# Performance work log

Measured on AMD Instinct MI355X. Metric: run time of the kernel, lower is better.

Reference implementation:

```python
import jax, jax.numpy as jnp
import numpy as np

N0, N1, N2, N3 = 1_000_000, 300_000, 80_000, 30_000
CIN, C = 4, 64  # in_channels, INIT_DIM / PLANES[0]
K = 27          # 3x3x3 octree kernel
EPS = 1e-5      # BatchNorm eps


def octree_conv(x, neigh, W):
    """Octree sparse conv as gather + GEMM.
    x: [Nin, Cin], neigh: [Nout, K] int indices into x, W: [K, Cin, Cout].
    """
    g = x[neigh]                              # [Nout, K, Cin] irregular gather
    return jnp.einsum('nkc,kcd->nd', g, W)    # [Nout, Cout]


def batchnorm(x, gamma, beta):
    # BatchNorm1d in training mode: batch stats over node dim, biased variance
    m = jnp.mean(x, axis=0)
    v = jnp.var(x, axis=0)
    return (x - m) * jax.lax.rsqrt(v + EPS) * gamma + beta


def setup_inputs() -> dict:
    key = jax.random.key(0)
    ks = jax.random.split(key, 16)
    s = 0.05
    return {
        'x': jax.random.normal(ks[0], (N0, CIN), jnp.float32),
        'neigh_stem': jax.random.randint(ks[1], (N1, K), 0, N0, jnp.int32),
        'pool_child': jax.random.randint(ks[2], (N2, 8), 0, N1, jnp.int32),
        'neigh_ds': jax.random.randint(ks[3], (N3, K), 0, N2, jnp.int32),
        'neigh_res': jax.random.randint(ks[4], (N3, K), 0, N3, jnp.int32),
        'W_stem': jax.random.normal(ks[5], (K, CIN, C), jnp.float32) * s,
        'g_stem': jnp.ones((C,), jnp.float32),
        'b_stem': jnp.zeros((C,), jnp.float32),
        'W1': jax.random.normal(ks[6], (K, C, C), jnp.float32) * s,
        'g1': jnp.ones((C,), jnp.float32),
        'b1': jnp.zeros((C,), jnp.float32),
        'W2': jax.random.normal(ks[7], (K, C, C), jnp.float32) * s,
        'g2': jnp.ones((C,), jnp.float32),
        'b2': jnp.zeros((C,), jnp.float32),
        'Wd': jax.random.normal(ks[8], (K, C, C), jnp.float32) * s,
        'gd': jnp.ones((C,), jnp.float32),
        'bd': jnp.zeros((C,), jnp.float32),
    }


def reference(x, neigh_stem, pool_child, neigh_ds, neigh_res,
              W_stem, g_stem, b_stem, W1, g1, b1, W2, g2, b2, Wd, gd, bd):
    # StemLayer: conv(s2) -> BN -> ReLU -> OctreeMaxPool
    h = jax.nn.relu(batchnorm(octree_conv(x, neigh_stem, W_stem), g_stem, b_stem))  # [N1, C]
    h = jnp.max(h[pool_child], axis=1)                                              # [N2, C]
    # ResBlock stride=2 (layer1, blocks=1)
    out = jax.nn.relu(batchnorm(octree_conv(h, neigh_ds, W1), g1, b1))              # [N3, C]
    out = batchnorm(octree_conv(out, neigh_res, W2), g2, b2)                        # [N3, C]
    residual = batchnorm(octree_conv(h, neigh_ds, Wd), gd, bd)                      # DownSample shortcut
    return jax.nn.relu(out + residual)
```

## Files before the change

kernel.cpp:

```cpp
#include <hip/hip_runtime.h>

constexpr int CN0 = 1000000;
constexpr int CN1 = 300000;
constexpr int CN2 = 80000;
constexpr int CN3 = 30000;
constexpr float BN_EPS = 1e-5f;

typedef __attribute__((ext_vector_type(8))) short bf16x8;
typedef __attribute__((ext_vector_type(4))) float f32x4;

union FragU { uint4 u; bf16x8 b; };

__device__ __forceinline__ float2 bn_ab(float s, float q, float invn, float gamma, float beta) {
  float m = s * invn;
  float v = fmaf(q, invn, -m * m);
  float rstd = rsqrtf(v + BN_EPS);
  float a = gamma * rstd;
  float b = beta - m * a;
  return make_float2(a, b);
}

__device__ __forceinline__ unsigned short f2bf(float f) {
  unsigned u = __float_as_uint(f);
  u += 0x7FFFu + ((u >> 16) & 1u);
  return (unsigned short)(u >> 16);
}

__device__ __forceinline__ void sync_lds() {
  asm volatile("s_waitcnt lgkmcnt(0)" ::: "memory");
  __builtin_amdgcn_s_barrier();
  asm volatile("" ::: "memory");
}

__global__ __launch_bounds__(256) void k_prep_x(
    const float* __restrict__ x, unsigned int* __restrict__ xbf) {
  int i = blockIdx.x * 256 + threadIdx.x;
  if (i >= CN0) return;
  float4 v = *(const float4*)(x + i * 4);
  uint2 p;
  p.x = (unsigned)f2bf(v.x) | ((unsigned)f2bf(v.y) << 16);
  p.y = (unsigned)f2bf(v.z) | ((unsigned)f2bf(v.w) << 16);
  *(uint2*)(xbf + i * 2) = p;
}

__global__ __launch_bounds__(256) void k_prep_stem(
    const float* __restrict__ W, unsigned short* __restrict__ Wt) {
  int f = blockIdx.x * 256 + threadIdx.x;
  if (f >= 8192) return;
  int e = f & 7, lane = (f >> 3) & 63, nf = (f >> 9) & 3, ks = f >> 11;
  int k = ks * 32 + (lane >> 4) * 8 + e;
  int d = nf * 16 + (lane & 15);
  Wt[f] = (k < 108) ? f2bf(W[k * 64 + d]) : (unsigned short)0;
}

__global__ __launch_bounds__(256) void k_prep_dual(
    const float* __restrict__ W1, const float* __restrict__ Wd,
    unsigned short* __restrict__ Wf) {
  int f = blockIdx.x * 256 + threadIdx.x;
  if (f >= 27 * 8192) return;
  int tap = f >> 13, r = f & 8191;
  int ks1 = (r >> 12) & 1, nfg = (r >> 9) & 7, lane = (r >> 3) & 63, e = r & 7;
  int cin = ks1 * 32 + (lane >> 4) * 8 + e;
  int d = nfg * 16 + (lane & 15);
  float v = (d < 64) ? W1[(tap * 64 + cin) * 64 + d]
                     : Wd[(tap * 64 + cin) * 64 + (d - 64)];
  Wf[f] = f2bf(v);
}

__global__ __launch_bounds__(256) void k_prep_res(
    const float* __restrict__ W2, unsigned short* __restrict__ Wf) {
  int f = blockIdx.x * 256 + threadIdx.x;
  if (f >= 27 * 4096) return;
  int tap = f >> 12, r = f & 4095;
  int ks1 = (r >> 11) & 1, nfg = (r >> 9) & 3, lane = (r >> 3) & 63, e = r & 7;
  int cin = ks1 * 32 + (lane >> 4) * 8 + e;
  int d = nfg * 16 + (lane & 15);
  Wf[f] = f2bf(W2[(tap * 64 + cin) * 64 + d]);
}

__global__ __launch_bounds__(256) void k_stem_mfma(
    const unsigned short* __restrict__ xbf, const int* __restrict__ neigh,
    const unsigned short* __restrict__ Wf, unsigned short* __restrict__ y1,
    float* __restrict__ stats) {
  __shared__ __align__(16) uint4 Bb[1024];
  const int tid = threadIdx.x;
  const int lane = tid & 63;
  const int wv = tid >> 6;
  const int l15 = lane & 15, lq = lane >> 4;
  const int g0 = blockIdx.x * 2;

  uint4 wreg[4];
  {
    const uint4* Ws = (const uint4*)Wf;
#pragma unroll
    for (int j = 0; j < 4; ++j) wreg[j] = Ws[tid + j * 256];
  }

  int idx0[8], idx1[8];
#define LDIDX(g, dst)                                                      \
  {                                                                        \
    int node_ = (g)*64 + wv * 16 + l15;                                    \
    bool rowok_ = node_ < CN1;                                             \
    const int* nb_ = neigh + node_ * 27;                                   \
    _Pragma("unroll") for (int ks_ = 0; ks_ < 4; ++ks_) {                  \
      int tap0_ = ks_ * 8 + lq * 2;                                        \
      dst[ks_ * 2] = (rowok_ && tap0_ < 27) ? nb_[tap0_] : -1;             \
      dst[ks_ * 2 + 1] = (rowok_ && tap0_ + 1 < 27) ? nb_[tap0_ + 1] : -1; \
    }                                                                      \
  }
#define GATHER(idx, frag)                                                  \
  {                                                                        \
    _Pragma("unroll") for (int ks_ = 0; ks_ < 4; ++ks_) {                  \
      uint2 v0_ = {0u, 0u}, v1_ = {0u, 0u};                                \
      if (idx[ks_ * 2] >= 0)                                               \
        v0_ = *(const uint2*)(xbf + idx[ks_ * 2] * 4);                     \
      if (idx[ks_ * 2 + 1] >= 0)                                           \
        v1_ = *(const uint2*)(xbf + idx[ks_ * 2 + 1] * 4);                 \
      frag[ks_].u.x = v0_.x; frag[ks_].u.y = v0_.y;                        \
      frag[ks_].u.z = v1_.x; frag[ks_].u.w = v1_.y;                        \
    }                                                                      \
  }

  LDIDX(g0 + 0, idx0);
  LDIDX(g0 + 1, idx1);
  FragU fA[4], fB[4];
  GATHER(idx0, fA);
  GATHER(idx1, fB);

#pragma unroll
  for (int j = 0; j < 4; ++j) Bb[tid + j * 256] = wreg[j];
  sync_lds();

  float sacc[4] = {0.f, 0.f, 0.f, 0.f};
  float qacc[4] = {0.f, 0.f, 0.f, 0.f};

#pragma unroll
  for (int t = 0; t < 2; ++t) {
    FragU* cur = t ? fB : fA;
    f32x4 acc[4] = {};
#pragma unroll
    for (int ks = 0; ks < 4; ++ks) {
#pragma unroll
      for (int nf = 0; nf < 4; ++nf) {
        bf16x8 b = *(const bf16x8*)&Bb[(ks * 4 + nf) * 64 + lane];
        acc[nf] = __builtin_amdgcn_mfma_f32_16x16x32_bf16(cur[ks].b, b,
                                                          acc[nf], 0, 0, 0);
      }
    }
    int n0 = (g0 + t) * 64 + wv * 16;
#pragma unroll
    for (int nf = 0; nf < 4; ++nf) {
      int c = nf * 16 + l15;
#pragma unroll
      for (int r = 0; r < 4; ++r) {
        int row = n0 + lq * 4 + r;
        float v = acc[nf][r];
        if (row < CN1) y1[row * 64 + c] = f2bf(v);
        sacc[nf] += v;
        qacc[nf] = fmaf(v, v, qacc[nf]);
      }
    }
  }
#undef LDIDX
#undef GATHER

  sync_lds();
  float* S = (float*)Bb;
#pragma unroll
  for (int nf = 0; nf < 4; ++nf) {
    float s = sacc[nf], q = qacc[nf];
    s += __shfl_xor(s, 16); s += __shfl_xor(s, 32);
    q += __shfl_xor(q, 16); q += __shfl_xor(q, 32);
    if (lane < 16) {
      S[wv * 64 + nf * 16 + lane] = s;
      S[256 + wv * 64 + nf * 16 + lane] = q;
    }
  }
  __syncthreads();
  if (tid < 64) {
    float s = S[tid] + S[64 + tid] + S[128 + tid] + S[192 + tid];
    float q = S[256 + tid] + S[320 + tid] + S[384 + tid] + S[448 + tid];
    atomicAdd(&stats[tid], s);
    atomicAdd(&stats[64 + tid], q);
  }
}

__global__ __launch_bounds__(256) void k_pool(
    const unsigned int* __restrict__ y1, const int* __restrict__ child,
    const float* __restrict__ stats, const float* __restrict__ gamma,
    const float* __restrict__ beta, unsigned int* __restrict__ h2) {
  const int tid = threadIdx.x;
  const int wd = tid & 31;
  const int n = blockIdx.x * 8 + (tid >> 5);
  const int c0 = wd * 2, c1 = c0 + 1;
  const int* crow = child + n * 8;
  int ch[8];
#pragma unroll
  for (int j = 0; j < 8; ++j) ch[j] = crow[j];
  unsigned vv[8];
#pragma unroll
  for (int j = 0; j < 8; ++j) vv[j] = y1[ch[j] * 32 + wd];

  float2 ab0 = bn_ab(stats[c0], stats[64 + c0], 1.0f / CN1, gamma[c0], beta[c0]);
  float2 ab1 = bn_ab(stats[c1], stats[64 + c1], 1.0f / CN1, gamma[c1], beta[c1]);
  float mx0 = -INFINITY, mn0 = INFINITY, mx1 = -INFINITY, mn1 = INFINITY;
#pragma unroll
  for (int j = 0; j < 8; ++j) {
    float v0 = __uint_as_float(vv[j] << 16);
    float v1 = __uint_as_float(vv[j] & 0xFFFF0000u);
    mx0 = fmaxf(mx0, v0); mn0 = fminf(mn0, v0);
    mx1 = fmaxf(mx1, v1); mn1 = fminf(mn1, v1);
  }
  float t0 = (ab0.x > 0.f) ? fmaf(ab0.x, mx0, ab0.y) : fmaf(ab0.x, mn0, ab0.y);
  float t1 = (ab1.x > 0.f) ? fmaf(ab1.x, mx1, ab1.y) : fmaf(ab1.x, mn1, ab1.y);
  unsigned o = (unsigned)f2bf(fmaxf(t0, 0.f)) |
               ((unsigned)f2bf(fmaxf(t1, 0.f)) << 16);
  h2[n * 32 + wd] = o;
}

template <int OUTC>
__global__ __launch_bounds__(OUTC * 2) void k_mconv(
    const unsigned short* __restrict__ src, const int* __restrict__ neigh,
    const unsigned short* __restrict__ Wf, float* __restrict__ out,
    float* __restrict__ stats, int M) {
  constexpr int CG = OUTC / 64;
  constexpr int PT = CG * 512;
  constexpr int K1 = 4 * CG;

  const int tid = threadIdx.x;
  const int lane = tid & 63;
  const int w = tid >> 6;
  const int ng = w & 1, cg = w >> 1;
  const int l15 = lane & 15, lq = lane >> 4;
  const int node = blockIdx.x * 32 + ng * 16 + l15;
  const bool ok = node < M;
  const int* myn = neigh + node * 27;
  const uint4* WfU = (const uint4*)Wf;
  const int cg4 = cg * 4;

  int i0 = -1, i1 = -1, i2 = -1, i3 = -1, i4 = -1, i5 = -1, i6 = -1,
      i7 = -1, i8 = -1, i9 = -1, i10 = -1, i11 = -1, i12 = -1, i13 = -1,
      i14 = -1, i15 = -1, i16 = -1, i17 = -1, i18 = -1, i19 = -1, i20 = -1,
      i21 = -1, i22 = -1, i23 = -1, i24 = -1, i25 = -1, i26 = -1;
  if (ok) {
    i0 = myn[0];   i1 = myn[1];   i2 = myn[2];   i3 = myn[3];
    i4 = myn[4];   i5 = myn[5];   i6 = myn[6];   i7 = myn[7];
    i8 = myn[8];   i9 = myn[9];   i10 = myn[10]; i11 = myn[11];
    i12 = myn[12]; i13 = myn[13]; i14 = myn[14]; i15 = myn[15];
    i16 = myn[16]; i17 = myn[17]; i18 = myn[18]; i19 = myn[19];
    i20 = myn[20]; i21 = myn[21]; i22 = myn[22]; i23 = myn[23];
    i24 = myn[24]; i25 = myn[25]; i26 = myn[26];
  }

  FragU a0l, a0h, a1l, a1h, a2l, a2h;
  FragU qa0, qa1, qa2, qa3, qa4, qa5, qa6, qa7;
  FragU qb0, qb1, qb2, qb3, qb4, qb5, qb6, qb7;
  f32x4 acc0 = {0.f, 0.f, 0.f, 0.f};
  f32x4 acc1 = {0.f, 0.f, 0.f, 0.f};
  f32x4 acc2 = {0.f, 0.f, 0.f, 0.f};
  f32x4 acc3 = {0.f, 0.f, 0.f, 0.f};

#define GATH2(AL, AH, ix)                                                  \
  {                                                                        \
    int ix_ = (ix);                                                        \
    if (ix_ >= 0) {                                                        \
      const char* bp_ = (const char*)src + (size_t)ix_ * 128 + lq * 16;    \
      AL.u = *(const uint4*)bp_;                                           \
      AH.u = *(const uint4*)(bp_ + 64);                                    \
    } else {                                                               \
      AL.u = uint4{0u, 0u, 0u, 0u};                                        \
      AH.u = uint4{0u, 0u, 0u, 0u};                                        \
    }                                                                      \
  }

#define LDB(QP, k)                                                         \
  {                                                                        \
    const uint4* bp_ = WfU + ((k)*PT + cg4 * 64 + lane);                   \
    (QP##0).u = bp_[0];                                                    \
    (QP##1).u = bp_[64];                                                   \
    (QP##2).u = bp_[128];                                                  \
    (QP##3).u = bp_[192];                                                  \
    (QP##4).u = bp_[K1 * 64];                                              \
    (QP##5).u = bp_[K1 * 64 + 64];                                         \
    (QP##6).u = bp_[K1 * 64 + 128];                                        \
    (QP##7).u = bp_[K1 * 64 + 192];                                        \
  }

#define MM(AP, QP)                                                            \
  acc0 = __builtin_amdgcn_mfma_f32_16x16x32_bf16((AP##l).b, (QP##0).b, acc0, 0, 0, 0); \
  acc0 = __builtin_amdgcn_mfma_f32_16x16x32_bf16((AP##h).b, (QP##4).b, acc0, 0, 0, 0); \
  acc1 = __builtin_amdgcn_mfma_f32_16x16x32_bf16((AP##l).b, (QP##1).b, acc1, 0, 0, 0); \
  acc1 = __builtin_amdgcn_mfma_f32_16x16x32_bf16((AP##h).b, (QP##5).b, acc1, 0, 0, 0); \
  acc2 = __builtin_amdgcn_mfma_f32_16x16x32_bf16((AP##l).b, (QP##2).b, acc2, 0, 0, 0); \
  acc2 = __builtin_amdgcn_mfma_f32_16x16x32_bf16((AP##h).b, (QP##6).b, acc2, 0, 0, 0); \
  acc3 = __builtin_amdgcn_mfma_f32_16x16x32_bf16((AP##l).b, (QP##3).b, acc3, 0, 0, 0); \
  acc3 = __builtin_amdgcn_mfma_f32_16x16x32_bf16((AP##h).b, (QP##7).b, acc3, 0, 0, 0);

#define TAP(k, AP, QP, QN, INX)          \
  {                                      \
    if ((k) + 1 < 27) LDB(QN, (k) + 1)   \
    MM(AP, QP)                           \
    if ((k) + 3 < 27) GATH2(AP##l, AP##h, INX) \
  }

  GATH2(a0l, a0h, i0)
  GATH2(a1l, a1h, i1)
  GATH2(a2l, a2h, i2)
  LDB(qa, 0)

  TAP(0, a0, qa, qb, i3)
  TAP(1, a1, qb, qa, i4)
  TAP(2, a2, qa, qb, i5)
  TAP(3, a0, qb, qa, i6)
  TAP(4, a1, qa, qb, i7)
  TAP(5, a2, qb, qa, i8)
  TAP(6, a0, qa, qb, i9)
  TAP(7, a1, qb, qa, i10)
  TAP(8, a2, qa, qb, i11)
  TAP(9, a0, qb, qa, i12)
  TAP(10, a1, qa, qb, i13)
  TAP(11, a2, qb, qa, i14)
  TAP(12, a0, qa, qb, i15)
  TAP(13, a1, qb, qa, i16)
  TAP(14, a2, qa, qb, i17)
  TAP(15, a0, qb, qa, i18)
  TAP(16, a1, qa, qb, i19)
  TAP(17, a2, qb, qa, i20)
  TAP(18, a0, qa, qb, i21)
  TAP(19, a1, qb, qa, i22)
  TAP(20, a2, qa, qb, i23)
  TAP(21, a0, qb, qa, i24)
  TAP(22, a1, qa, qb, i25)
  TAP(23, a2, qb, qa, i26)
  TAP(24, a0, qa, qb, i0)
  TAP(25, a1, qb, qa, i0)
  TAP(26, a2, qa, qb, i0)
#undef TAP
#undef MM
#undef LDB
#undef GATH2

  const int rowbase = blockIdx.x * 32 + ng * 16 + lq * 4;
#pragma unroll
  for (int nf = 0; nf < 4; ++nf) {
    f32x4 a = (nf == 0) ? acc0 : (nf == 1) ? acc1 : (nf == 2) ? acc2 : acc3;
    int c = cg * 64 + nf * 16 + l15;
#pragma unroll
    for (int r = 0; r < 4; ++r) {
      int row = rowbase + r;
      if (row < M) out[row * OUTC + c] = a[r];
    }
  }

#pragma unroll
  for (int nf = 0; nf < 4; ++nf) {
    f32x4 a = (nf == 0) ? acc0 : (nf == 1) ? acc1 : (nf == 2) ? acc2 : acc3;
    float s = 0.f, q = 0.f;
#pragma unroll
    for (int r = 0; r < 4; ++r) {
      float v = a[r];
      s += v; q += v * v;
    }
    s += __shfl_xor(s, 16); s += __shfl_xor(s, 32);
    q += __shfl_xor(q, 16); q += __shfl_xor(q, 32);
    if (lane < 16) {
      int c = cg * 64 + nf * 16 + lane;
      atomicAdd(&stats[c], s);
      atomicAdd(&stats[OUTC + c], q);
    }
  }
}

__global__ __launch_bounds__(256) void k_bnrelu(
    const float* __restrict__ y2d, const float* __restrict__ stats,
    const float* __restrict__ gamma, const float* __restrict__ beta,
    unsigned short* __restrict__ out1) {
  int e = blockIdx.x * 256 + threadIdx.x;
  int i = e >> 6, c = e & 63;
  float2 ab = bn_ab(stats[c], stats[128 + c], 1.0f / CN3, gamma[c], beta[c]);
  out1[e] = f2bf(fmaxf(fmaf(ab.x, y2d[i * 128 + c], ab.y), 0.f));
}

__global__ __launch_bounds__(256) void k_final(
    const float* __restrict__ y3, const float* __restrict__ y2d,
    const float* __restrict__ stats2, const float* __restrict__ stats1d,
    const float* __restrict__ g2, const float* __restrict__ b2,
    const float* __restrict__ gd, const float* __restrict__ bd,
    float* __restrict__ dout) {
  int e = blockIdx.x * 256 + threadIdx.x;
  int i = e >> 6, c = e & 63;
  float2 ab2 = bn_ab(stats2[c], stats2[64 + c], 1.0f / CN3, g2[c], b2[c]);
  float2 abd =
      bn_ab(stats1d[64 + c], stats1d[192 + c], 1.0f / CN3, gd[c], bd[c]);
  float o = fmaf(ab2.x, y3[e], ab2.y) + fmaf(abd.x, y2d[i * 128 + 64 + c], abd.y);
  dout[e] = fmaxf(o, 0.f);
}

extern "C" void kernel_launch(void* const* d_in, const int* in_sizes, int n_in,
                              void* d_out, int out_size, void* d_ws,
                              size_t ws_size, hipStream_t stream) {
  const float* x = (const float*)d_in[0];
  const int* neigh_stem = (const int*)d_in[1];
  const int* pool_child = (const int*)d_in[2];
  const int* neigh_ds = (const int*)d_in[3];
  const int* neigh_res = (const int*)d_in[4];
  const float* W_stem = (const float*)d_in[5];
  const float* g_stem = (const float*)d_in[6];
  const float* b_stem = (const float*)d_in[7];
  const float* W1 = (const float*)d_in[8];
  const float* g1 = (const float*)d_in[9];
  const float* b1 = (const float*)d_in[10];
  const float* W2 = (const float*)d_in[11];
  const float* g2 = (const float*)d_in[12];
  const float* b2 = (const float*)d_in[13];
  const float* Wd = (const float*)d_in[14];
  const float* gd = (const float*)d_in[15];
  const float* bd = (const float*)d_in[16];
  float* out = (float*)d_out;
  float* ws = (float*)d_ws;

  unsigned short* y1bf = (unsigned short*)ws;
  float* y2d = ws;
  unsigned short* out1bf = (unsigned short*)(ws + 3840000);
  float* y3 = ws + 4800000;
  unsigned short* h2bf = (unsigned short*)(ws + 9600000);
  unsigned int* xbf = (unsigned int*)(ws + 12160000);
  unsigned short* Wst = (unsigned short*)(ws + 14160000);
  unsigned short* Wdual = (unsigned short*)(ws + 14164096);
  unsigned short* Wres = (unsigned short*)(ws + 14274688);
  float* stats = ws + 14329984;
  float* stats_stem = stats;
  float* stats_1d = stats + 128;
  float* stats_2 = stats + 384;

  hipMemsetAsync(stats, 0, 512 * sizeof(float), stream);

  k_prep_x<<<(CN0 + 255) / 256, 256, 0, stream>>>(x, xbf);
  k_prep_stem<<<(8192 + 255) / 256, 256, 0, stream>>>(W_stem, Wst);
  k_prep_dual<<<(27 * 8192 + 255) / 256, 256, 0, stream>>>(W1, Wd, Wdual);
  k_prep_res<<<(27 * 4096 + 255) / 256, 256, 0, stream>>>(W2, Wres);

  k_stem_mfma<<<2344, 256, 0, stream>>>(
      (const unsigned short*)xbf, neigh_stem, Wst, y1bf, stats_stem);
  k_pool<<<CN2 / 8, 256, 0, stream>>>((const unsigned int*)y1bf, pool_child,
                                      stats_stem, g_stem, b_stem,
                                      (unsigned int*)h2bf);
  k_mconv<128><<<(CN3 + 31) / 32, 256, 0, stream>>>(h2bf, neigh_ds, Wdual,
                                                    y2d, stats_1d, CN3);
  k_bnrelu<<<CN3 * 64 / 256, 256, 0, stream>>>(y2d, stats_1d, g1, b1, out1bf);
  k_mconv<64><<<(CN3 + 31) / 32, 128, 0, stream>>>(out1bf, neigh_res, Wres,
                                                   y3, stats_2, CN3);
  k_final<<<CN3 * 64 / 256, 256, 0, stream>>>(y3, y2d, stats_2, stats_1d, g2,
                                              b2, gd, bd, out);
}
```

Before: 292.4 us.

## Process more rows per block in stem and mconv, stage neighbor indices in LDS

The stem conv kernel now handles four 64-row groups per block instead of two, with a software pipeline that gathers the next group and loads indices two groups ahead while the current group computes. The weight tile is written straight into LDS at the start. The mconv kernel now covers 64 nodes per block with two accumulator sets, so each loaded weight fragment feeds twice as many MFMAs. Its neighbor indices are staged cooperatively in LDS rather than kept in 27 registers per thread. This halves the weight reloads and block count, at the cost of more registers, fewer blocks for latency hiding, and an LDS index read on every gather.

```diff
diff --git a/kernel.cpp b/kernel.cpp
--- a/kernel.cpp
+++ b/kernel.cpp
@@ -82,61 +82,65 @@
     const unsigned short* __restrict__ xbf, const int* __restrict__ neigh,
     const unsigned short* __restrict__ Wf, unsigned short* __restrict__ y1,
     float* __restrict__ stats) {
+  constexpr int T = 4;
   __shared__ __align__(16) uint4 Bb[1024];
   const int tid = threadIdx.x;
   const int lane = tid & 63;
   const int wv = tid >> 6;
   const int l15 = lane & 15, lq = lane >> 4;
-  const int g0 = blockIdx.x * 2;
-
-  uint4 wreg[4];
+  const int g0 = blockIdx.x * T;
+
   {
-    const uint4* Ws = (const uint4*)Wf;
-#pragma unroll
-    for (int j = 0; j < 4; ++j) wreg[j] = Ws[tid + j * 256];
-  }
-
-  int idx0[8], idx1[8];
-#define LDIDX(g, dst)                                                      \
-  {                                                                        \
-    int node_ = (g)*64 + wv * 16 + l15;                                    \
-    bool rowok_ = node_ < CN1;                                             \
-    const int* nb_ = neigh + node_ * 27;                                   \
-    _Pragma("unroll") for (int ks_ = 0; ks_ < 4; ++ks_) {                  \
-      int tap0_ = ks_ * 8 + lq * 2;                                        \
-      dst[ks_ * 2] = (rowok_ && tap0_ < 27) ? nb_[tap0_] : -1;             \
+    const uint4* Wsrc = (const uint4*)Wf;
+#pragma unroll
+    for (int j = 0; j < 4; ++j) Bb[tid + j * 256] = Wsrc[tid + j * 256];
+  }
+  __syncthreads();
+
+  int idxA[8], idxB[8];
+  FragU fragA[4], fragB[4];
+
+#define LDIDX(g, dst)                                                   \
+  {                                                                     \
+    int node_ = (g)*64 + wv * 16 + l15;                                 \
+    bool rowok_ = node_ < CN1;                                          \
+    const int* nb_ = neigh + node_ * 27;                                \
+    _Pragma("unroll") for (int ks_ = 0; ks_ < 4; ++ks_) {               \
+      int tap0_ = ks_ * 8 + lq * 2;                                     \
+      dst[ks_ * 2] = (rowok_ && tap0_ < 27) ? nb_[tap0_] : -1;          \
       dst[ks_ * 2 + 1] = (rowok_ && tap0_ + 1 < 27) ? nb_[tap0_ + 1] : -1; \
-    }                                                                      \
-  }
-#define GATHER(idx, frag)                                                  \
-  {                                                                        \
-    _Pragma("unroll") for (int ks_ = 0; ks_ < 4; ++ks_) {                  \
-      uint2 v0_ = {0u, 0u}, v1_ = {0u, 0u};                                \
-      if (idx[ks_ * 2] >= 0)                                               \
-        v0_ = *(const uint2*)(xbf + idx[ks_ * 2] * 4);                     \
-      if (idx[ks_ * 2 + 1] >= 0)                                           \
-        v1_ = *(const uint2*)(xbf + idx[ks_ * 2 + 1] * 4);                 \
-      frag[ks_].u.x = v0_.x; frag[ks_].u.y = v0_.y;                        \
-      frag[ks_].u.z = v1_.x; frag[ks_].u.w = v1_.y;                        \
-    }                                                                      \
-  }
-
-  LDIDX(g0 + 0, idx0);
-  LDIDX(g0 + 1, idx1);
-  FragU fA[4], fB[4];
-  GATHER(idx0, fA);
-  GATHER(idx1, fB);
-
-#pragma unroll
-  for (int j = 0; j < 4; ++j) Bb[tid + j * 256] = wreg[j];
-  sync_lds();
+    }                                                                   \
+  }
+
+#define GATHER(idx, frag)                                               \
+  {                                                                     \
+    _Pragma("unroll") for (int ks_ = 0; ks_ < 4; ++ks_) {               \
+      uint2 v0_ = {0u, 0u}, v1_ = {0u, 0u};                             \
+      if (idx[ks_ * 2] >= 0)                                            \
+        v0_ = *(const uint2*)(xbf + idx[ks_ * 2] * 4);                  \
+      if (idx[ks_ * 2 + 1] >= 0)                                        \
+        v1_ = *(const uint2*)(xbf + idx[ks_ * 2 + 1] * 4);              \
+      frag[ks_].u.x = v0_.x; frag[ks_].u.y = v0_.y;                     \
+      frag[ks_].u.z = v1_.x; frag[ks_].u.w = v1_.y;                     \
+    }                                                                   \
+  }
+
+  LDIDX(0 + g0, idxA);
+  GATHER(idxA, fragA);
+  LDIDX(1 + g0, idxB);
 
   float sacc[4] = {0.f, 0.f, 0.f, 0.f};
   float qacc[4] = {0.f, 0.f, 0.f, 0.f};
 
 #pragma unroll
-  for (int t = 0; t < 2; ++t) {
-    FragU* cur = t ? fB : fA;
+  for (int t = 0; t < T; ++t) {
+    FragU* cur = (t & 1) ? fragB : fragA;
+    FragU* nxt = (t & 1) ? fragA : fragB;
+    int* idn = (t & 1) ? idxA : idxB;
+    int* idn2 = (t & 1) ? idxB : idxA;
+    if (t + 1 < T) GATHER(idn, nxt);
+    if (t + 2 < T) LDIDX(g0 + t + 2, idn2);
+
     f32x4 acc[4] = {};
 #pragma unroll
     for (int ks = 0; ks < 4; ++ks) {
@@ -147,6 +151,7 @@
                                                           acc[nf], 0, 0, 0);
       }
     }
+
     int n0 = (g0 + t) * 64 + wv * 16;
 #pragma unroll
     for (int nf = 0; nf < 4; ++nf) {
@@ -164,7 +169,7 @@
 #undef LDIDX
 #undef GATHER
 
-  sync_lds();
+  __syncthreads();
   float* S = (float*)Bb;
 #pragma unroll
   for (int nf = 0; nf < 4; ++nf) {
@@ -224,41 +229,47 @@
     const unsigned short* __restrict__ Wf, float* __restrict__ out,
     float* __restrict__ stats, int M) {
   constexpr int CG = OUTC / 64;
+  constexpr int THREADS = OUTC * 2;
   constexpr int PT = CG * 512;
   constexpr int K1 = 4 * CG;
+  __shared__ int nlds[64 * 27];
 
   const int tid = threadIdx.x;
   const int lane = tid & 63;
   const int w = tid >> 6;
   const int ng = w & 1, cg = w >> 1;
   const int l15 = lane & 15, lq = lane >> 4;
-  const int node = blockIdx.x * 32 + ng * 16 + l15;
-  const bool ok = node < M;
-  const int* myn = neigh + node * 27;
   const uint4* WfU = (const uint4*)Wf;
   const int cg4 = cg * 4;
-
-  int i0 = -1, i1 = -1, i2 = -1, i3 = -1, i4 = -1, i5 = -1, i6 = -1,
-      i7 = -1, i8 = -1, i9 = -1, i10 = -1, i11 = -1, i12 = -1, i13 = -1,
-      i14 = -1, i15 = -1, i16 = -1, i17 = -1, i18 = -1, i19 = -1, i20 = -1,
-      i21 = -1, i22 = -1, i23 = -1, i24 = -1, i25 = -1, i26 = -1;
-  if (ok) {
-    i0 = myn[0];   i1 = myn[1];   i2 = myn[2];   i3 = myn[3];
-    i4 = myn[4];   i5 = myn[5];   i6 = myn[6];   i7 = myn[7];
-    i8 = myn[8];   i9 = myn[9];   i10 = myn[10]; i11 = myn[11];
-    i12 = myn[12]; i13 = myn[13]; i14 = myn[14]; i15 = myn[15];
-    i16 = myn[16]; i17 = myn[17]; i18 = myn[18]; i19 = myn[19];
-    i20 = myn[20]; i21 = myn[21]; i22 = myn[22]; i23 = myn[23];
-    i24 = myn[24]; i25 = myn[25]; i26 = myn[26];
-  }
-
-  FragU a0l, a0h, a1l, a1h, a2l, a2h;
+  const int offA = (ng * 32 + l15) * 27;
+  const int offB = offA + 16 * 27;
+
+  for (int e = tid; e < 64 * 27; e += THREADS) {
+    int row = blockIdx.x * 64 + e / 27;
+    nlds[e] = (row < M) ? neigh[row * 27 + e % 27] : -1;
+  }
+
+  FragU x0l, x0h, x1l, x1h, x2l, x2h;
+  FragU y0l, y0h, y1l, y1h, y2l, y2h;
   FragU qa0, qa1, qa2, qa3, qa4, qa5, qa6, qa7;
   FragU qb0, qb1, qb2, qb3, qb4, qb5, qb6, qb7;
-  f32x4 acc0 = {0.f, 0.f, 0.f, 0.f};
-  f32x4 acc1 = {0.f, 0.f, 0.f, 0.f};
-  f32x4 acc2 = {0.f, 0.f, 0.f, 0.f};
-  f32x4 acc3 = {0.f, 0.f, 0.f, 0.f};
+  f32x4 ca0 = {0.f, 0.f, 0.f, 0.f}, ca1 = {0.f, 0.f, 0.f, 0.f};
+  f32x4 ca2 = {0.f, 0.f, 0.f, 0.f}, ca3 = {0.f, 0.f, 0.f, 0.f};
+  f32x4 cb0 = {0.f, 0.f, 0.f, 0.f}, cb1 = {0.f, 0.f, 0.f, 0.f};
+  f32x4 cb2 = {0.f, 0.f, 0.f, 0.f}, cb3 = {0.f, 0.f, 0.f, 0.f};
+
+#define LDB(QP, k)                                                         \
+  {                                                                        \
+    const uint4* bp_ = WfU + ((k)*PT + cg4 * 64 + lane);                   \
+    (QP##0).u = bp_[0];                                                    \
+    (QP##1).u = bp_[64];                                                   \
+    (QP##2).u = bp_[128];                                                  \
+    (QP##3).u = bp_[192];                                                  \
+    (QP##4).u = bp_[K1 * 64];                                              \
+    (QP##5).u = bp_[K1 * 64 + 64];                                         \
+    (QP##6).u = bp_[K1 * 64 + 128];                                        \
+    (QP##7).u = bp_[K1 * 64 + 192];                                        \
+  }
 
 #define GATH2(AL, AH, ix)                                                  \
   {                                                                        \
@@ -273,93 +284,92 @@
     }                                                                      \
   }
 
-#define LDB(QP, k)                                                         \
-  {                                                                        \
-    const uint4* bp_ = WfU + ((k)*PT + cg4 * 64 + lane);                   \
-    (QP##0).u = bp_[0];                                                    \
-    (QP##1).u = bp_[64];                                                   \
-    (QP##2).u = bp_[128];                                                  \
-    (QP##3).u = bp_[192];                                                  \
-    (QP##4).u = bp_[K1 * 64];                                              \
-    (QP##5).u = bp_[K1 * 64 + 64];                                         \
-    (QP##6).u = bp_[K1 * 64 + 128];                                        \
-    (QP##7).u = bp_[K1 * 64 + 192];                                        \
-  }
-
-#define MM(AP, QP)                                                            \
-  acc0 = __builtin_amdgcn_mfma_f32_16x16x32_bf16((AP##l).b, (QP##0).b, acc0, 0, 0, 0); \
-  acc0 = __builtin_amdgcn_mfma_f32_16x16x32_bf16((AP##h).b, (QP##4).b, acc0, 0, 0, 0); \
-  acc1 = __builtin_amdgcn_mfma_f32_16x16x32_bf16((AP##l).b, (QP##1).b, acc1, 0, 0, 0); \
-  acc1 = __builtin_amdgcn_mfma_f32_16x16x32_bf16((AP##h).b, (QP##5).b, acc1, 0, 0, 0); \
-  acc2 = __builtin_amdgcn_mfma_f32_16x16x32_bf16((AP##l).b, (QP##2).b, acc2, 0, 0, 0); \
-  acc2 = __builtin_amdgcn_mfma_f32_16x16x32_bf16((AP##h).b, (QP##6).b, acc2, 0, 0, 0); \
-  acc3 = __builtin_amdgcn_mfma_f32_16x16x32_bf16((AP##l).b, (QP##3).b, acc3, 0, 0, 0); \
-  acc3 = __builtin_amdgcn_mfma_f32_16x16x32_bf16((AP##h).b, (QP##7).b, acc3, 0, 0, 0);
-
-#define TAP(k, AP, QP, QN, INX)          \
-  {                                      \
-    if ((k) + 1 < 27) LDB(QN, (k) + 1)   \
-    MM(AP, QP)                           \
-    if ((k) + 3 < 27) GATH2(AP##l, AP##h, INX) \
-  }
-
-  GATH2(a0l, a0h, i0)
-  GATH2(a1l, a1h, i1)
-  GATH2(a2l, a2h, i2)
+#define MMG(AL, AH, C0, C1, C2, C3, QP)                                       \
+  C0 = __builtin_amdgcn_mfma_f32_16x16x32_bf16((AL).b, (QP##0).b, C0, 0, 0, 0); \
+  C1 = __builtin_amdgcn_mfma_f32_16x16x32_bf16((AL).b, (QP##1).b, C1, 0, 0, 0); \
+  C2 = __builtin_amdgcn_mfma_f32_16x16x32_bf16((AL).b, (QP##2).b, C2, 0, 0, 0); \
+  C3 = __builtin_amdgcn_mfma_f32_16x16x32_bf16((AL).b, (QP##3).b, C3, 0, 0, 0); \
+  C0 = __builtin_amdgcn_mfma_f32_16x16x32_bf16((AH).b, (QP##4).b, C0, 0, 0, 0); \
+  C1 = __builtin_amdgcn_mfma_f32_16x16x32_bf16((AH).b, (QP##5).b, C1, 0, 0, 0); \
+  C2 = __builtin_amdgcn_mfma_f32_16x16x32_bf16((AH).b, (QP##6).b, C2, 0, 0, 0); \
+  C3 = __builtin_amdgcn_mfma_f32_16x16x32_bf16((AH).b, (QP##7).b, C3, 0, 0, 0);
+
+#define TAP(k, XL, XH, YL, YH, QP, QN)                 \
+  {                                                    \
+    if ((k) + 1 < 27) LDB(QN, (k) + 1)                 \
+    MMG(XL, XH, ca0, ca1, ca2, ca3, QP)                \
+    MMG(YL, YH, cb0, cb1, cb2, cb3, QP)                \
+    if ((k) + 3 < 27) {                                \
+      GATH2(XL, XH, nlds[offA + (k) + 3])              \
+      GATH2(YL, YH, nlds[offB + (k) + 3])              \
+    }                                                  \
+  }
+
   LDB(qa, 0)
-
-  TAP(0, a0, qa, qb, i3)
-  TAP(1, a1, qb, qa, i4)
-  TAP(2, a2, qa, qb, i5)
-  TAP(3, a0, qb, qa, i6)
-  TAP(4, a1, qa, qb, i7)
-  TAP(5, a2, qb, qa, i8)
-  TAP(6, a0, qa, qb, i9)
-  TAP(7, a1, qb, qa, i10)
-  TAP(8, a2, qa, qb, i11)
-  TAP(9, a0, qb, qa, i12)
-  TAP(10, a1, qa, qb, i13)
-  TAP(11, a2, qb, qa, i14)
-  TAP(12, a0, qa, qb, i15)
-  TAP(13, a1, qb, qa, i16)
-  TAP(14, a2, qa, qb, i17)
-  TAP(15, a0, qb, qa, i18)
-  TAP(16, a1, qa, qb, i19)
-  TAP(17, a2, qb, qa, i20)
-  TAP(18, a0, qa, qb, i21)
-  TAP(19, a1, qb, qa, i22)
-  TAP(20, a2, qa, qb, i23)
-  TAP(21, a0, qb, qa, i24)
-  TAP(22, a1, qa, qb, i25)
-  TAP(23, a2, qb, qa, i26)
-  TAP(24, a0, qa, qb, i0)
-  TAP(25, a1, qb, qa, i0)
-  TAP(26, a2, qa, qb, i0)
+  sync_lds();
+
+  GATH2(x0l, x0h, nlds[offA + 0])
+  GATH2(y0l, y0h, nlds[offB + 0])
+  GATH2(x1l, x1h, nlds[offA + 1])
+  GATH2(y1l, y1h, nlds[offB + 1])
+  GATH2(x2l, x2h, nlds[offA + 2])
+  GATH2(y2l, y2h, nlds[offB + 2])
+
+  TAP(0, x0l, x0h, y0l, y0h, qa, qb)
+  TAP(1, x1l, x1h, y1l, y1h, qb, qa)
+  TAP(2, x2l, x2h, y2l, y2h, qa, qb)
+  TAP(3, x0l, x0h, y0l, y0h, qb, qa)
+  TAP(4, x1l, x1h, y1l, y1h, qa, qb)
+  TAP(5, x2l, x2h, y2l, y2h, qb, qa)
+  TAP(6, x0l, x0h, y0l, y0h, qa, qb)
+  TAP(7, x1l, x1h, y1l, y1h, qb, qa)
+  TAP(8, x2l, x2h, y2l, y2h, qa, qb)
+  TAP(9, x0l, x0h, y0l, y0h, qb, qa)
+  TAP(10, x1l, x1h, y1l, y1h, qa, qb)
+  TAP(11, x2l, x2h, y2l, y2h, qb, qa)
+  TAP(12, x0l, x0h, y0l, y0h, qa, qb)
+  TAP(13, x1l, x1h, y1l, y1h, qb, qa)
+  TAP(14, x2l, x2h, y2l, y2h, qa, qb)
+  TAP(15, x0l, x0h, y0l, y0h, qb, qa)
+  TAP(16, x1l, x1h, y1l, y1h, qa, qb)
+  TAP(17, x2l, x2h, y2l, y2h, qb, qa)
+  TAP(18, x0l, x0h, y0l, y0h, qa, qb)
+  TAP(19, x1l, x1h, y1l, y1h, qb, qa)
+  TAP(20, x2l, x2h, y2l, y2h, qa, qb)
+  TAP(21, x0l, x0h, y0l, y0h, qb, qa)
+  TAP(22, x1l, x1h, y1l, y1h, qa, qb)
+  TAP(23, x2l, x2h, y2l, y2h, qb, qa)
+  TAP(24, x0l, x0h, y0l, y0h, qa, qb)
+  TAP(25, x1l, x1h, y1l, y1h, qb, qa)
+  TAP(26, x2l, x2h, y2l, y2h, qa, qb)
 #undef TAP
-#undef MM
+#undef MMG
+#undef GATH2
 #undef LDB
-#undef GATH2
-
-  const int rowbase = blockIdx.x * 32 + ng * 16 + lq * 4;
+
+  const int rbA = blockIdx.x * 64 + ng * 32 + lq * 4;
 #pragma unroll
   for (int nf = 0; nf < 4; ++nf) {
-    f32x4 a = (nf == 0) ? acc0 : (nf == 1) ? acc1 : (nf == 2) ? acc2 : acc3;
+    f32x4 a = (nf == 0) ? ca0 : (nf == 1) ? ca1 : (nf == 2) ? ca2 : ca3;
+    f32x4 b = (nf == 0) ? cb0 : (nf == 1) ? cb1 : (nf == 2) ? cb2 : cb3;
     int c = cg * 64 + nf * 16 + l15;
 #pragma unroll
     for (int r = 0; r < 4; ++r) {
-      int row = rowbase + r;
-      if (row < M) out[row * OUTC + c] = a[r];
+      int rowA = rbA + r, rowB = rbA + 16 + r;
+      if (rowA < M) out[rowA * OUTC + c] = a[r];
+      if (rowB < M) out[rowB * OUTC + c] = b[r];
     }
   }
 
 #pragma unroll
   for (int nf = 0; nf < 4; ++nf) {
-    f32x4 a = (nf == 0) ? acc0 : (nf == 1) ? acc1 : (nf == 2) ? acc2 : acc3;
+    f32x4 a = (nf == 0) ? ca0 : (nf == 1) ? ca1 : (nf == 2) ? ca2 : ca3;
+    f32x4 b = (nf == 0) ? cb0 : (nf == 1) ? cb1 : (nf == 2) ? cb2 : cb3;
     float s = 0.f, q = 0.f;
 #pragma unroll
     for (int r = 0; r < 4; ++r) {
-      float v = a[r];
-      s += v; q += v * v;
+      s += a[r] + b[r];
+      q += a[r] * a[r] + b[r] * b[r];
     }
     s += __shfl_xor(s, 16); s += __shfl_xor(s, 32);
     q += __shfl_xor(q, 16); q += __shfl_xor(q, 32);
@@ -440,15 +450,15 @@
   k_prep_dual<<<(27 * 8192 + 255) / 256, 256, 0, stream>>>(W1, Wd, Wdual);
   k_prep_res<<<(27 * 4096 + 255) / 256, 256, 0, stream>>>(W2, Wres);
 
-  k_stem_mfma<<<2344, 256, 0, stream>>>(
+  k_stem_mfma<<<1172, 256, 0, stream>>>(
       (const unsigned short*)xbf, neigh_stem, Wst, y1bf, stats_stem);
   k_pool<<<CN2 / 8, 256, 0, stream>>>((const unsigned int*)y1bf, pool_child,
                                       stats_stem, g_stem, b_stem,
                                       (unsigned int*)h2bf);
-  k_mconv<128><<<(CN3 + 31) / 32, 256, 0, stream>>>(h2bf, neigh_ds, Wdual,
+  k_mconv<128><<<(CN3 + 63) / 64, 256, 0, stream>>>(h2bf, neigh_ds, Wdual,
                                                     y2d, stats_1d, CN3);
   k_bnrelu<<<CN3 * 64 / 256, 256, 0, stream>>>(y2d, stats_1d, g1, b1, out1bf);
-  k_mconv<64><<<(CN3 + 31) / 32, 128, 0, stream>>>(out1bf, neigh_res, Wres,
+  k_mconv<64><<<(CN3 + 63) / 64, 128, 0, stream>>>(out1bf, neigh_res, Wres,
                                                    y3, stats_2, CN3);
   k_final<<<CN3 * 64 / 256, 256, 0, stream>>>(y3, y2d, stats_2, stats_1d, g2,
                                               b2, gd, bd, out);
```

Result: faster. 239.1 us (-18.3%).
